# Optimization experiments

Measured on AMD Instinct MI355X. Metric: run time of the kernel, lower is better.

Reference implementation:

```python
import jax, jax.numpy as jnp
import numpy as np

B, QL, D = 4, 1024, 1024
H, HD = 16, 64
KVL = 2048


def setup_inputs() -> dict:
    key = jax.random.key(0)
    ks = jax.random.split(key, 6)
    scale = 1.0 / np.sqrt(D)
    return {
        "hidden_states": jax.random.normal(ks[0], (B, QL, D), dtype=jnp.float32),
        "key_states": jax.random.normal(ks[1], (B, H, KVL, HD), dtype=jnp.float32),
        "value_states": jax.random.normal(ks[2], (B, H, KVL, HD), dtype=jnp.float32),
        "attention_mask": jnp.zeros((B, 1, 1, KVL), dtype=jnp.float32),
        "Wq": jax.random.normal(ks[3], (D, D), dtype=jnp.float32) * scale,
        "Wo": jax.random.normal(ks[4], (D, D), dtype=jnp.float32) * scale,
    }


def reference(hidden_states, key_states, value_states, attention_mask, Wq, Wo):
    batch = hidden_states.shape[0]
    # Q projection (T5 Linear has no bias), split heads: [B, H, Q, HD]
    q = jnp.einsum("bqd,de->bqe", hidden_states, Wq)
    q = q.reshape(batch, -1, H, HD).transpose(0, 2, 1, 3)
    # NOTE: T5 attention has NO 1/sqrt(d) scaling
    scores = jnp.einsum("bhqd,bhkd->bhqk", q, key_states) + attention_mask
    attn = jax.nn.softmax(scores.astype(jnp.float32), axis=-1).astype(scores.dtype)
    out = jnp.einsum("bhqk,bhkd->bhqd", attn, value_states)
    out = out.transpose(0, 2, 1, 3).reshape(batch, -1, H * HD)
    return jnp.einsum("bqe,ed->bqd", out, Wo)
```

## Files before the change

kernel.cpp:

```cpp
#include <hip/hip_runtime.h>
#include <hip/hip_bf16.h>
#include <hip/hip_fp16.h>
#include <stdint.h>

typedef _Float16 f16;
typedef _Float16 f16x2 __attribute__((ext_vector_type(2)));
typedef _Float16 f16x4 __attribute__((ext_vector_type(4)));
typedef _Float16 f16x8 __attribute__((ext_vector_type(8)));
typedef float f32x4 __attribute__((ext_vector_type(4)));
typedef float f32x16 __attribute__((ext_vector_type(16)));

#define B_ 4
#define QL_ 1024
#define D_ 1024
#define H_ 16
#define HD_ 64
#define KVL_ 2048
#define L2E 1.44269504088896f

__device__ __forceinline__ void g2lds16(const void* g, void* l) {
    __builtin_amdgcn_global_load_lds(
        (const __attribute__((address_space(1))) uint32_t*)g,
        (__attribute__((address_space(3))) uint32_t*)l,
        16, 0, 0);
}

union U8 { uint32_t u[4]; f16x8 v; };

__device__ __forceinline__ uint32_t pkrtz(float a, float b) {
    auto t = __builtin_amdgcn_cvt_pkrtz(a, b);
    return __builtin_bit_cast(uint32_t, t);
}

__global__ void preprocess(const float* __restrict__ hs, f16* __restrict__ hs_h,
                           const float* __restrict__ K, f16* __restrict__ K_h,
                           const float* __restrict__ Wq, f16* __restrict__ Wq_t,
                           const float* __restrict__ Wo, f16* __restrict__ Wo_t,
                           const float* __restrict__ V, f16* __restrict__ V_t,
                           const float* __restrict__ mask, float* __restrict__ mL) {
    __shared__ float t[64][65];
    int bid = blockIdx.x, tid = threadIdx.x;
    if (bid < 2048) {
        const int n4a = (B_ * QL_ * D_) / 4;
        const int n4b = (B_ * H_ * KVL_ * HD_) / 4;
        int i = bid * 256 + tid;
        int st = 2048 * 256;
        for (; i < n4a + n4b; i += st) {
            float4 v = (i < n4a) ? ((const float4*)hs)[i] : ((const float4*)K)[i - n4a];
            f16x4 o = { (f16)v.x, (f16)v.y, (f16)v.z, (f16)v.w };
            if (i < n4a) ((f16x4*)hs_h)[i] = o; else ((f16x4*)K_h)[i - n4a] = o;
        }
    } else if (bid < 2560) {
        int wbid = bid - 2048;
        const float* src = wbid < 256 ? Wq : Wo;
        f16* dst = wbid < 256 ? Wq_t : Wo_t;
        int b2 = wbid & 255;
        int k0 = (b2 >> 4) << 6, n0 = (b2 & 15) << 6;
        int rr = tid >> 4, c4 = (tid & 15) << 2;
#pragma unroll
        for (int i = 0; i < 4; ++i) {
            int r = i * 16 + rr;
            float4 v = *(const float4*)(src + (size_t)(k0 + r) * 1024 + n0 + c4);
            t[r][c4 + 0] = v.x; t[r][c4 + 1] = v.y; t[r][c4 + 2] = v.z; t[r][c4 + 3] = v.w;
        }
        __syncthreads();
#pragma unroll
        for (int i = 0; i < 4; ++i) {
            int n = i * 16 + rr;
            f16x4 o;
#pragma unroll
            for (int j = 0; j < 4; ++j) o[j] = (f16)t[c4 + j][n];
            *(f16x4*)(dst + (size_t)(n0 + n) * 1024 + k0 + c4) = o;
        }
    } else if (bid < 4608) {
        int vbid = bid - 2560;
        int bh = vbid >> 5, kv0 = (vbid & 31) << 6;
        int rr = tid >> 4, c4 = (tid & 15) << 2;
        const int permq[4] = {0, 2, 1, 3};
        int pc4 = (c4 & ~15) + permq[(c4 >> 2) & 3] * 4;
#pragma unroll
        for (int i = 0; i < 4; ++i) {
            int r = i * 16 + rr;
            float4 v = *(const float4*)(V + ((size_t)bh * KVL_ + kv0 + r) * HD_ + c4);
            t[r][c4 + 0] = v.x; t[r][c4 + 1] = v.y; t[r][c4 + 2] = v.z; t[r][c4 + 3] = v.w;
        }
        __syncthreads();
#pragma unroll
        for (int i = 0; i < 4; ++i) {
            int d = i * 16 + rr;
            f16x4 o;
#pragma unroll
            for (int j = 0; j < 4; ++j) o[j] = (f16)t[c4 + j][d];
            *(f16x4*)(V_t + ((size_t)bh * HD_ + d) * KVL_ + kv0 + pc4) = o;
        }
    } else {
        int i = (bid - 4608) * 256 + tid;
        if (i < (B_ * KVL_) / 4) {
            f32x4 v = ((const f32x4*)mask)[i];
            v *= L2E;
            ((f32x4*)mL)[i] = v;
        }
    }
}

template <int EPI>
__global__ __launch_bounds__(512) void gemm_tn(
    const f16* __restrict__ A, const f16* __restrict__ BT, void* __restrict__ Cout,
    int M, int N, int K) {
    __shared__ char Alds[2][16384];
    __shared__ char Blds[2][8192];
    int d0 = blockIdx.x;
    int xcd = d0 & 7, sx = d0 >> 3;
    int bm = xcd * 4 + (sx & 3);
    int bn = sx >> 2;
    int tid = threadIdx.x, w = tid >> 6, l = tid & 63;
    int l15 = l & 15, lg = l >> 4;
    int wm = w >> 1, wn = w & 1;
    f32x4 acc[2][2] = {};

    const char* ag[2]; int ao[2];
#pragma unroll
    for (int jj = 0; jj < 2; ++jj) {
        int instr = w + 8 * jj;
        int r = instr * 8 + (l >> 3);
        int cc = (l & 7) ^ (r & 7);
        ag[jj] = (const char*)A + ((size_t)(bm * 128 + r) * K + cc * 8) * 2;
        ao[jj] = instr * 1024;
    }
    int rB = w * 8 + (l >> 3);
    int ccB = (l & 7) ^ (rB & 7);
    const char* bgp = (const char*)BT + ((size_t)(bn * 64 + rB) * K + ccB * 8) * 2;
    int boB = w * 1024;

#define GSTAGE(buf, kt)                                       \
    {                                                         \
        g2lds16(ag[0] + (size_t)(kt) * 128, &Alds[buf][ao[0]]); \
        g2lds16(ag[1] + (size_t)(kt) * 128, &Alds[buf][ao[1]]); \
        g2lds16(bgp + (size_t)(kt) * 128, &Blds[buf][boB]);     \
    }

    int nk = K >> 6;
    GSTAGE(0, 0);
    asm volatile("s_waitcnt vmcnt(0)" ::: "memory");
    __syncthreads();

    for (int kt = 0; kt < nk; ++kt) {
        int cur = kt & 1;
        if (kt + 1 < nk) GSTAGE(cur ^ 1, kt + 1);
#pragma unroll
        for (int ks = 0; ks < 2; ++ks) {
            f16x8 af[2], bf[2];
#pragma unroll
            for (int m = 0; m < 2; ++m) {
                int r = wm * 32 + m * 16 + l15;
                af[m] = *(const f16x8*)(&Alds[cur][r * 128 + ((ks * 64 + lg * 16) ^ ((r & 7) << 4))]);
            }
#pragma unroll
            for (int n = 0; n < 2; ++n) {
                int r = wn * 32 + n * 16 + l15;
                bf[n] = *(const f16x8*)(&Blds[cur][r * 128 + ((ks * 64 + lg * 16) ^ ((r & 7) << 4))]);
            }
#pragma unroll
            for (int m = 0; m < 2; ++m)
#pragma unroll
                for (int n = 0; n < 2; ++n)
                    acc[m][n] = __builtin_amdgcn_mfma_f32_16x16x32_f16(af[m], bf[n], acc[m][n], 0, 0, 0);
        }
        asm volatile("s_waitcnt vmcnt(0)" ::: "memory");
        __syncthreads();
    }

#pragma unroll
    for (int m = 0; m < 2; ++m)
#pragma unroll
        for (int n = 0; n < 2; ++n)
#pragma unroll
            for (int i = 0; i < 4; ++i) {
                int row = bm * 128 + wm * 32 + m * 16 + lg * 4 + i;
                int col = bn * 64 + wn * 32 + n * 16 + l15;
                if (EPI == 0) {
                    float v = acc[m][n][i] * L2E;
                    int b = row >> 10, q = row & 1023, h = col >> 6, d = col & 63;
                    ((f16*)Cout)[(((size_t)b * H_ + h) * QL_ + q) * HD_ + d] = (f16)v;
                } else {
                    ((float*)Cout)[(size_t)row * N + col] = acc[m][n][i];
                }
            }
#undef GSTAGE
}

__global__ __launch_bounds__(512, 4) void attn_fused(
    const f16* __restrict__ qh, const f16* __restrict__ kh, const f16* __restrict__ vt,
    const float* __restrict__ mL, f16* __restrict__ aout) {
    __shared__ char lds_buf[65536];
    __shared__ float frl[8][32];
    __shared__ float fr2[4][2][32];
    __shared__ float2 msx[4][32];

    int tid = threadIdx.x, w = tid >> 6, l = tid & 63;
    int l31 = l & 31, hi = l >> 5;
    int swl = (l31 & 7) << 4;
    int g = w >> 2, wg = w & 3;
    int d0 = blockIdx.x;
    int xcd = d0 & 7, sx = d0 >> 3;
    int bh = xcd * 8 + (sx & 7);
    int qt = sx >> 3;
    int b = bh >> 4, h = bh & 15;

    char* Kst = lds_buf + g * 32768;
    char* Vst = lds_buf + g * 32768 + 16384;

    f16x8 Qf[4];
    {
        const f16* qp = qh + ((size_t)bh * QL_ + qt * 128 + wg * 32 + l31) * HD_ + hi * 8;
#pragma unroll
        for (int ds_ = 0; ds_ < 4; ++ds_) Qf[ds_] = *(const f16x8*)(qp + ds_ * 16);
    }

    const char* kg0; const char* vg0; int ko0, vo0;
    {
        int instr = wg;
        int r = instr * 8 + (l >> 3);
        int cc = (l & 7) ^ (r & 7);
        kg0 = (const char*)kh + ((size_t)bh * KVL_ + g * 1024 + r) * 128 + cc * 16;
        ko0 = instr * 1024;
        vg0 = (const char*)vt + ((size_t)bh * HD_ + r) * (KVL_ * 2) + g * 2048 + cc * 16;
        vo0 = instr * 1024;
    }

#define ASTAGE(buf, ch)                                                              \
    {                                                                                \
        g2lds16(kg0 + (size_t)(ch) * 8192, Kst + (buf) * 8192 + ko0);                \
        g2lds16(kg0 + (size_t)(ch) * 8192 + 4096, Kst + (buf) * 8192 + ko0 + 4096);  \
        g2lds16(vg0 + (size_t)(ch) * 128, Vst + (buf) * 8192 + vo0);                 \
        g2lds16(vg0 + (size_t)(ch) * 128 + 131072, Vst + (buf) * 8192 + vo0 + 4096); \
    }

    float mrun = -1e30f, ssum = 0.f;
    f32x16 acc[2] = {};
    const float* mpb = mL + b * KVL_ + g * 1024;
    const f16x2 one2 = { (f16)1.0f, (f16)1.0f };

    ASTAGE(0, 0);
    asm volatile("s_waitcnt vmcnt(0)" ::: "memory");
    __syncthreads();

    for (int ch = 0; ch < 16; ++ch) {
        int cur = ch & 1;
        if (ch + 1 < 16) ASTAGE(cur ^ 1, ch + 1);
        const char* Kc = Kst + cur * 8192;
        const char* Vc = Vst + cur * 8192;

#pragma unroll
        for (int kb = 0; kb < 2; ++kb) {
            f32x16 St;
#pragma unroll
            for (int g4 = 0; g4 < 4; ++g4) {
                f32x4 mv = *(const f32x4*)(mpb + ch * 64 + kb * 32 + g4 * 8 + hi * 4);
                St[g4 * 4 + 0] = mv[0]; St[g4 * 4 + 1] = mv[1];
                St[g4 * 4 + 2] = mv[2]; St[g4 * 4 + 3] = mv[3];
            }
            __builtin_amdgcn_s_setprio(1);
#pragma unroll
            for (int ds_ = 0; ds_ < 4; ++ds_) {
                f16x8 kf = *(const f16x8*)(Kc + (kb * 32 + l31) * 128 + ((ds_ * 32 + hi * 16) ^ swl));
                St = __builtin_amdgcn_mfma_f32_32x32x16_f16(kf, Qf[ds_], St, 0, 0, 0);
            }
            __builtin_amdgcn_s_setprio(0);

            float a0 = fmaxf(fmaxf(St[0], St[1]), St[2]);
            float a1 = fmaxf(fmaxf(St[3], St[4]), St[5]);
            float a2 = fmaxf(fmaxf(St[6], St[7]), St[8]);
            float a3 = fmaxf(fmaxf(St[9], St[10]), St[11]);
            float a4 = fmaxf(fmaxf(St[12], St[13]), St[14]);
            float pm = fmaxf(fmaxf(fmaxf(a0, a1), St[15]), fmaxf(fmaxf(a2, a3), a4));
            pm = fmaxf(pm, __shfl_xor(pm, 32));

            if (__any(pm > mrun + 12.f)) {
                float mn = fmaxf(mrun, pm);
                float fac = exp2f(mrun - mn);
                mrun = mn;
                ssum *= fac;
                frl[w][l31] = fac;
                asm volatile("s_waitcnt lgkmcnt(0)" ::: "memory");
#pragma unroll
                for (int g4 = 0; g4 < 4; ++g4) {
                    f32x4 fv = *(const f32x4*)&frl[w][g4 * 8 + hi * 4];
#pragma unroll
                    for (int c = 0; c < 2; ++c)
#pragma unroll
                        for (int j = 0; j < 4; ++j) acc[c][g4 * 4 + j] *= fv[j];
                }
            }

            uint32_t pk[8];
#pragma unroll
            for (int i = 0; i < 8; ++i) {
                float p0 = exp2f(St[2 * i] - mrun);
                float p1 = exp2f(St[2 * i + 1] - mrun);
                uint32_t u = pkrtz(p0, p1);
                pk[i] = u;
                ssum = __builtin_amdgcn_fdot2(__builtin_bit_cast(f16x2, u), one2, ssum, false);
            }

            __builtin_amdgcn_s_setprio(1);
#pragma unroll
            for (int sti = 0; sti < 2; ++sti) {
                U8 pa;
                pa.u[0] = pk[sti * 4 + 0]; pa.u[1] = pk[sti * 4 + 1];
                pa.u[2] = pk[sti * 4 + 2]; pa.u[3] = pk[sti * 4 + 3];
                int st_ = kb * 2 + sti;
#pragma unroll
                for (int c = 0; c < 2; ++c) {
                    U8 vb;
                    vb.v = *(const f16x8*)(Vc + (c * 32 + l31) * 128 + ((st_ * 32 + hi * 16) ^ swl));
                    acc[c] = __builtin_amdgcn_mfma_f32_32x32x16_f16(pa.v, vb.v, acc[c], 0, 0, 0);
                }
            }
            __builtin_amdgcn_s_setprio(0);
        }
        asm volatile("s_waitcnt vmcnt(0)" ::: "memory");
        __syncthreads();
    }

    ssum += __shfl_xor(ssum, 32);
    char* exch = lds_buf;
    if (g == 1) {
        int base = (wg * 64 + l) * 128;
#pragma unroll
        for (int i = 0; i < 8; ++i) {
            int c = i >> 2, j0 = (i & 3) * 4;
            f32x4 vv = { acc[c][j0], acc[c][j0 + 1], acc[c][j0 + 2], acc[c][j0 + 3] };
            *(f32x4*)(exch + base + ((i * 16) ^ ((l & 7) << 4))) = vv;
        }
        if (hi == 0) msx[wg][l31] = make_float2(mrun, ssum);
    }
    __syncthreads();
    if (g == 0) {
        float2 mb = msx[wg][l31];
        float m = fmaxf(mrun, mb.x);
        float fA = exp2f(mrun - m), fB = exp2f(mb.x - m);
        float s = ssum * fA + mb.y * fB;
        float rinv = 1.0f / s;
        if (hi == 0) { fr2[wg][0][l31] = fA * rinv; fr2[wg][1][l31] = fB * rinv; }
        asm volatile("s_waitcnt lgkmcnt(0)" ::: "memory");
        int base = (wg * 64 + l) * 128;
#pragma unroll
        for (int c = 0; c < 2; ++c)
#pragma unroll
            for (int g4 = 0; g4 < 4; ++g4) {
                f32x4 gAv = *(const f32x4*)&fr2[wg][0][g4 * 8 + hi * 4];
                f32x4 gBv = *(const f32x4*)&fr2[wg][1][g4 * 8 + hi * 4];
                int i = c * 4 + g4;
                f32x4 pv = *(const f32x4*)(exch + base + ((i * 16) ^ ((l & 7) << 4)));
#pragma unroll
                for (int j = 0; j < 4; ++j) {
                    float o = acc[c][g4 * 4 + j] * gAv[j] + pv[j] * gBv[j];
                    int q = qt * 128 + wg * 32 + g4 * 8 + hi * 4 + j;
                    int dd = c * 32 + l31;
                    aout[((size_t)b * QL_ + q) * D_ + h * HD_ + dd] = (f16)o;
                }
            }
    }
#undef ASTAGE
}

extern "C" void kernel_launch(void* const* d_in, const int* in_sizes, int n_in,
                              void* d_out, int out_size, void* d_ws, size_t ws_size,
                              hipStream_t stream) {
    const float* hs = (const float*)d_in[0];
    const float* K  = (const float*)d_in[1];
    const float* V  = (const float*)d_in[2];
    const float* mask = (const float*)d_in[3];
    const float* Wq = (const float*)d_in[4];
    const float* Wo = (const float*)d_in[5];
    float* out = (float*)d_out;
    char* ws = (char*)d_ws;

    f16* hs_h = (f16*)(ws + 0);
    f16* Wq_t = (f16*)(ws + 8388608);
    f16* Wo_t = (f16*)(ws + 10485760);
    f16* K_h  = (f16*)(ws + 12582912);
    f16* V_t  = (f16*)(ws + 29360128);
    f16* q_h  = (f16*)(ws + 46137344);
    f16* a_o  = (f16*)(ws + 54525952);
    float* mL = (float*)(ws + 62914560);

    preprocess<<<4616, 256, 0, stream>>>(hs, hs_h, K, K_h, Wq, Wq_t, Wo, Wo_t,
                                         V, V_t, mask, mL);
    gemm_tn<0><<<512, 512, 0, stream>>>(hs_h, Wq_t, (void*)q_h, 4096, 1024, 1024);
    attn_fused<<<512, 512, 0, stream>>>(q_h, K_h, V_t, mL, a_o);
    gemm_tn<1><<<512, 512, 0, stream>>>(a_o, Wo_t, (void*)out, 4096, 1024, 1024);
}
```

Before: 117.6 us.

## Pre-swizzle K and V into fragment-ordered layout; unroll GEMM and attention loops

```diff
diff --git a/kernel.cpp b/kernel.cpp
--- a/kernel.cpp
+++ b/kernel.cpp
@@ -40,18 +40,30 @@
                            const float* __restrict__ mask, float* __restrict__ mL) {
     __shared__ float t[64][65];
     int bid = blockIdx.x, tid = threadIdx.x;
-    if (bid < 2048) {
-        const int n4a = (B_ * QL_ * D_) / 4;
-        const int n4b = (B_ * H_ * KVL_ * HD_) / 4;
-        int i = bid * 256 + tid;
-        int st = 2048 * 256;
-        for (; i < n4a + n4b; i += st) {
-            float4 v = (i < n4a) ? ((const float4*)hs)[i] : ((const float4*)K)[i - n4a];
+    if (bid < 1024) {
+        const int n4 = (B_ * QL_ * D_) / 4;
+        for (int i = bid * 256 + tid; i < n4; i += 1024 * 256) {
+            float4 v = ((const float4*)hs)[i];
             f16x4 o = { (f16)v.x, (f16)v.y, (f16)v.z, (f16)v.w };
-            if (i < n4a) ((f16x4*)hs_h)[i] = o; else ((f16x4*)K_h)[i - n4a] = o;
-        }
-    } else if (bid < 2560) {
-        int wbid = bid - 2048;
+            ((f16x4*)hs_h)[i] = o;
+        }
+    } else if (bid < 3072) {
+        int t0 = (bid - 1024) * 256 + tid;
+#pragma unroll
+        for (int rep = 0; rep < 2; ++rep) {
+            int U = t0 + rep * 524288;
+            int bh = U >> 14, rem = U & 16383;
+            int ch = rem >> 9, r2 = rem & 511;
+            int dsl = r2 >> 7, r3 = r2 & 127;
+            int kv = r3 >> 1, hi2 = r3 & 1;
+            const float* sp = K + (((size_t)bh * KVL_ + ch * 64 + kv) * HD_ + dsl * 16 + hi2 * 8);
+            f16x8 o;
+#pragma unroll
+            for (int j = 0; j < 8; ++j) o[j] = (f16)sp[j];
+            *(f16x8*)(K_h + (size_t)U * 8) = o;
+        }
+    } else if (bid < 3584) {
+        int wbid = bid - 3072;
         const float* src = wbid < 256 ? Wq : Wo;
         f16* dst = wbid < 256 ? Wq_t : Wo_t;
         int b2 = wbid & 255;
@@ -72,29 +84,31 @@
             for (int j = 0; j < 4; ++j) o[j] = (f16)t[c4 + j][n];
             *(f16x4*)(dst + (size_t)(n0 + n) * 1024 + k0 + c4) = o;
         }
-    } else if (bid < 4608) {
-        int vbid = bid - 2560;
-        int bh = vbid >> 5, kv0 = (vbid & 31) << 6;
+    } else if (bid < 5632) {
+        int vb = bid - 3584;
+        int bh = vb >> 5, ch = vb & 31;
         int rr = tid >> 4, c4 = (tid & 15) << 2;
-        const int permq[4] = {0, 2, 1, 3};
-        int pc4 = (c4 & ~15) + permq[(c4 >> 2) & 3] * 4;
 #pragma unroll
         for (int i = 0; i < 4; ++i) {
             int r = i * 16 + rr;
-            float4 v = *(const float4*)(V + ((size_t)bh * KVL_ + kv0 + r) * HD_ + c4);
+            float4 v = *(const float4*)(V + ((size_t)bh * KVL_ + ch * 64 + r) * HD_ + c4);
             t[r][c4 + 0] = v.x; t[r][c4 + 1] = v.y; t[r][c4 + 2] = v.z; t[r][c4 + 3] = v.w;
         }
         __syncthreads();
 #pragma unroll
-        for (int i = 0; i < 4; ++i) {
-            int d = i * 16 + rr;
-            f16x4 o;
-#pragma unroll
-            for (int j = 0; j < 4; ++j) o[j] = (f16)t[c4 + j][d];
-            *(f16x4*)(V_t + ((size_t)bh * HD_ + d) * KVL_ + kv0 + pc4) = o;
+        for (int rep = 0; rep < 2; ++rep) {
+            int u = tid + rep * 256;
+            int st = u >> 7, d = (u >> 1) & 63, hi2 = u & 1;
+            f16x8 o;
+#pragma unroll
+            for (int j = 0; j < 8; ++j) {
+                int kvl = st * 16 + (j & 3) + 8 * (j >> 2) + 4 * hi2;
+                o[j] = (f16)t[kvl][d];
+            }
+            *(f16x8*)(V_t + ((size_t)(bh * 32 + ch) * 512 + u) * 8) = o;
         }
     } else {
-        int i = (bid - 4608) * 256 + tid;
+        int i = (bid - 5632) * 256 + tid;
         if (i < (B_ * KVL_) / 4) {
             f32x4 v = ((const f32x4*)mask)[i];
             v *= L2E;
@@ -118,56 +132,65 @@
     int wm = w >> 1, wn = w & 1;
     f32x4 acc[2][2] = {};
 
-    const char* ag[2]; int ao[2];
-#pragma unroll
-    for (int jj = 0; jj < 2; ++jj) {
-        int instr = w + 8 * jj;
-        int r = instr * 8 + (l >> 3);
-        int cc = (l & 7) ^ (r & 7);
-        ag[jj] = (const char*)A + ((size_t)(bm * 128 + r) * K + cc * 8) * 2;
-        ao[jj] = instr * 1024;
+    const char* ag0; const char* ag1; int ao0, ao1;
+    {
+        int i0 = w, i1 = w + 8;
+        int r0 = i0 * 8 + (l >> 3), r1 = i1 * 8 + (l >> 3);
+        int c0 = (l & 7) ^ (r0 & 7), c1 = (l & 7) ^ (r1 & 7);
+        ag0 = (const char*)A + ((size_t)(bm * 128 + r0) * K + c0 * 8) * 2;
+        ag1 = (const char*)A + ((size_t)(bm * 128 + r1) * K + c1 * 8) * 2;
+        ao0 = i0 * 1024; ao1 = i1 * 1024;
     }
     int rB = w * 8 + (l >> 3);
     int ccB = (l & 7) ^ (rB & 7);
     const char* bgp = (const char*)BT + ((size_t)(bn * 64 + rB) * K + ccB * 8) * 2;
     int boB = w * 1024;
 
-#define GSTAGE(buf, kt)                                       \
-    {                                                         \
-        g2lds16(ag[0] + (size_t)(kt) * 128, &Alds[buf][ao[0]]); \
-        g2lds16(ag[1] + (size_t)(kt) * 128, &Alds[buf][ao[1]]); \
-        g2lds16(bgp + (size_t)(kt) * 128, &Blds[buf][boB]);     \
-    }
-
-    int nk = K >> 6;
+    int aoff[2][2], boff[2][2];
+#pragma unroll
+    for (int ks = 0; ks < 2; ++ks)
+#pragma unroll
+        for (int m = 0; m < 2; ++m) {
+            int ra = wm * 32 + m * 16 + l15;
+            aoff[ks][m] = ra * 128 + ((ks * 64 + lg * 16) ^ ((ra & 7) << 4));
+            int rb = wn * 32 + m * 16 + l15;
+            boff[ks][m] = rb * 128 + ((ks * 64 + lg * 16) ^ ((rb & 7) << 4));
+        }
+    const char* Ab = &Alds[0][0];
+    const char* Bb = &Blds[0][0];
+
+#define GSTAGE(buf, soff)                                      \
+    {                                                          \
+        g2lds16(ag0 + (soff), &Alds[buf][ao0]);                \
+        g2lds16(ag1 + (soff), &Alds[buf][ao1]);                \
+        g2lds16(bgp + (soff), &Blds[buf][boB]);                \
+    }
+#define GCOMP(buf)                                                               \
+    _Pragma("unroll") for (int ks = 0; ks < 2; ++ks) {                           \
+        f16x8 af[2], bf[2];                                                      \
+        af[0] = *(const f16x8*)(Ab + (buf) * 16384 + aoff[ks][0]);               \
+        af[1] = *(const f16x8*)(Ab + (buf) * 16384 + aoff[ks][1]);               \
+        bf[0] = *(const f16x8*)(Bb + (buf) * 8192 + boff[ks][0]);                \
+        bf[1] = *(const f16x8*)(Bb + (buf) * 8192 + boff[ks][1]);                \
+        _Pragma("unroll") for (int m = 0; m < 2; ++m)                            \
+            _Pragma("unroll") for (int n = 0; n < 2; ++n)                        \
+                acc[m][n] = __builtin_amdgcn_mfma_f32_16x16x32_f16(af[m], bf[n], acc[m][n], 0, 0, 0); \
+    }
+
     GSTAGE(0, 0);
     asm volatile("s_waitcnt vmcnt(0)" ::: "memory");
     __syncthreads();
 
-    for (int kt = 0; kt < nk; ++kt) {
-        int cur = kt & 1;
-        if (kt + 1 < nk) GSTAGE(cur ^ 1, kt + 1);
-#pragma unroll
-        for (int ks = 0; ks < 2; ++ks) {
-            f16x8 af[2], bf[2];
-#pragma unroll
-            for (int m = 0; m < 2; ++m) {
-                int r = wm * 32 + m * 16 + l15;
-                af[m] = *(const f16x8*)(&Alds[cur][r * 128 + ((ks * 64 + lg * 16) ^ ((r & 7) << 4))]);
-            }
-#pragma unroll
-            for (int n = 0; n < 2; ++n) {
-                int r = wn * 32 + n * 16 + l15;
-                bf[n] = *(const f16x8*)(&Blds[cur][r * 128 + ((ks * 64 + lg * 16) ^ ((r & 7) << 4))]);
-            }
-#pragma unroll
-            for (int m = 0; m < 2; ++m)
-#pragma unroll
-                for (int n = 0; n < 2; ++n)
-                    acc[m][n] = __builtin_amdgcn_mfma_f32_16x16x32_f16(af[m], bf[n], acc[m][n], 0, 0, 0);
-        }
+    for (int t2 = 0; t2 < 8; ++t2) {
+        GSTAGE(1, 128);
+        GCOMP(0);
         asm volatile("s_waitcnt vmcnt(0)" ::: "memory");
         __syncthreads();
+        if (t2 < 7) GSTAGE(0, 256);
+        GCOMP(1);
+        asm volatile("s_waitcnt vmcnt(0)" ::: "memory");
+        __syncthreads();
+        ag0 += 256; ag1 += 256; bgp += 256;
     }
 
 #pragma unroll
@@ -187,6 +210,7 @@
                 }
             }
 #undef GSTAGE
+#undef GCOMP
 }
 
 __global__ __launch_bounds__(512, 4) void attn_fused(
@@ -199,7 +223,6 @@
 
     int tid = threadIdx.x, w = tid >> 6, l = tid & 63;
     int l31 = l & 31, hi = l >> 5;
-    int swl = (l31 & 7) << 4;
     int g = w >> 2, wg = w & 3;
     int d0 = blockIdx.x;
     int xcd = d0 & 7, sx = d0 >> 3;
@@ -207,8 +230,7 @@
     int qt = sx >> 3;
     int b = bh >> 4, h = bh & 15;
 
-    char* Kst = lds_buf + g * 32768;
-    char* Vst = lds_buf + g * 32768 + 16384;
+    const char* lbase = lds_buf + g * 32768 + l31 * 32 + hi * 16;
 
     f16x8 Qf[4];
     {
@@ -217,110 +239,101 @@
         for (int ds_ = 0; ds_ < 4; ++ds_) Qf[ds_] = *(const f16x8*)(qp + ds_ * 16);
     }
 
-    const char* kg0; const char* vg0; int ko0, vo0;
-    {
-        int instr = wg;
-        int r = instr * 8 + (l >> 3);
-        int cc = (l & 7) ^ (r & 7);
-        kg0 = (const char*)kh + ((size_t)bh * KVL_ + g * 1024 + r) * 128 + cc * 16;
-        ko0 = instr * 1024;
-        vg0 = (const char*)vt + ((size_t)bh * HD_ + r) * (KVL_ * 2) + g * 2048 + cc * 16;
-        vo0 = instr * 1024;
-    }
-
-#define ASTAGE(buf, ch)                                                              \
-    {                                                                                \
-        g2lds16(kg0 + (size_t)(ch) * 8192, Kst + (buf) * 8192 + ko0);                \
-        g2lds16(kg0 + (size_t)(ch) * 8192 + 4096, Kst + (buf) * 8192 + ko0 + 4096);  \
-        g2lds16(vg0 + (size_t)(ch) * 128, Vst + (buf) * 8192 + vo0);                 \
-        g2lds16(vg0 + (size_t)(ch) * 128 + 131072, Vst + (buf) * 8192 + vo0 + 4096); \
+    int i0 = wg * 2;
+    const char* kgp0 = (const char*)kh + (((size_t)(bh * 32 + g * 16) * 512) + i0 * 64 + l) * 16;
+    const char* kgp1 = kgp0 + 1024;
+    const char* vgp0 = (const char*)vt + (((size_t)(bh * 32 + g * 16) * 512) + i0 * 64 + l) * 16;
+    const char* vgp1 = vgp0 + 1024;
+    char* kl0 = lds_buf + g * 32768 + i0 * 1024;
+    char* kl1 = kl0 + 1024;
+    char* vl0 = lds_buf + g * 32768 + 16384 + i0 * 1024;
+    char* vl1 = vl0 + 1024;
+
+#define PREF(buf, soff)                                  \
+    {                                                    \
+        g2lds16(kgp0 + (soff), kl0 + (buf) * 8192);      \
+        g2lds16(kgp1 + (soff), kl1 + (buf) * 8192);      \
+        g2lds16(vgp0 + (soff), vl0 + (buf) * 8192);      \
+        g2lds16(vgp1 + (soff), vl1 + (buf) * 8192);      \
     }
 
     float mrun = -1e30f, ssum = 0.f;
     f32x16 acc[2] = {};
-    const float* mpb = mL + b * KVL_ + g * 1024;
+    const float* mp = mL + b * KVL_ + g * 1024;
     const f16x2 one2 = { (f16)1.0f, (f16)1.0f };
 
-    ASTAGE(0, 0);
+#define BODY(buf, mo)                                                                     \
+    _Pragma("unroll") for (int kb = 0; kb < 2; ++kb) {                                    \
+        f32x16 St;                                                                        \
+        _Pragma("unroll") for (int g4 = 0; g4 < 4; ++g4) {                                \
+            f32x4 mv = *(const f32x4*)(mp + (mo) + kb * 32 + g4 * 8 + hi * 4);            \
+            St[g4 * 4 + 0] = mv[0]; St[g4 * 4 + 1] = mv[1];                               \
+            St[g4 * 4 + 2] = mv[2]; St[g4 * 4 + 3] = mv[3];                               \
+        }                                                                                 \
+        __builtin_amdgcn_s_setprio(1);                                                    \
+        _Pragma("unroll") for (int ds_ = 0; ds_ < 4; ++ds_) {                             \
+            f16x8 kf = *(const f16x8*)(lbase + (buf) * 8192 + ds_ * 2048 + kb * 1024);    \
+            St = __builtin_amdgcn_mfma_f32_32x32x16_f16(kf, Qf[ds_], St, 0, 0, 0);        \
+        }                                                                                 \
+        __builtin_amdgcn_s_setprio(0);                                                    \
+        float a0 = fmaxf(fmaxf(St[0], St[1]), St[2]);                                     \
+        float a1 = fmaxf(fmaxf(St[3], St[4]), St[5]);                                     \
+        float a2 = fmaxf(fmaxf(St[6], St[7]), St[8]);                                     \
+        float a3 = fmaxf(fmaxf(St[9], St[10]), St[11]);                                   \
+        float a4 = fmaxf(fmaxf(St[12], St[13]), St[14]);                                  \
+        float pm = fmaxf(fmaxf(fmaxf(a0, a1), St[15]), fmaxf(fmaxf(a2, a3), a4));         \
+        pm = fmaxf(pm, __shfl_xor(pm, 32));                                               \
+        if (__any(pm > mrun + 12.f)) {                                                    \
+            float mn = fmaxf(mrun, pm);                                                   \
+            float fac = exp2f(mrun - mn);                                                 \
+            mrun = mn; ssum *= fac;                                                       \
+            frl[w][l31] = fac;                                                            \
+            asm volatile("s_waitcnt lgkmcnt(0)" ::: "memory");                            \
+            _Pragma("unroll") for (int g4 = 0; g4 < 4; ++g4) {                            \
+                f32x4 fv = *(const f32x4*)&frl[w][g4 * 8 + hi * 4];                       \
+                _Pragma("unroll") for (int c = 0; c < 2; ++c)                             \
+                    _Pragma("unroll") for (int j = 0; j < 4; ++j)                         \
+                        acc[c][g4 * 4 + j] *= fv[j];                                      \
+            }                                                                             \
+        }                                                                                 \
+        uint32_t pk[8];                                                                   \
+        _Pragma("unroll") for (int i = 0; i < 8; ++i) {                                   \
+            float p0 = exp2f(St[2 * i] - mrun);                                           \
+            float p1 = exp2f(St[2 * i + 1] - mrun);                                       \
+            uint32_t u = pkrtz(p0, p1);                                                   \
+            pk[i] = u;                                                                    \
+            ssum = __builtin_amdgcn_fdot2(__builtin_bit_cast(f16x2, u), one2, ssum, false); \
+        }                                                                                 \
+        __builtin_amdgcn_s_setprio(1);                                                    \
+        _Pragma("unroll") for (int sti = 0; sti < 2; ++sti) {                             \
+            U8 pa;                                                                        \
+            pa.u[0] = pk[sti * 4 + 0]; pa.u[1] = pk[sti * 4 + 1];                         \
+            pa.u[2] = pk[sti * 4 + 2]; pa.u[3] = pk[sti * 4 + 3];                         \
+            const int st_ = kb * 2 + sti;                                                 \
+            _Pragma("unroll") for (int c = 0; c < 2; ++c) {                               \
+                U8 vb;                                                                    \
+                vb.v = *(const f16x8*)(lbase + 16384 + (buf) * 8192 + st_ * 2048 + c * 1024); \
+                acc[c] = __builtin_amdgcn_mfma_f32_32x32x16_f16(pa.v, vb.v, acc[c], 0, 0, 0); \
+            }                                                                             \
+        }                                                                                 \
+        __builtin_amdgcn_s_setprio(0);                                                    \
+    }
+
+    PREF(0, 0);
     asm volatile("s_waitcnt vmcnt(0)" ::: "memory");
     __syncthreads();
 
-    for (int ch = 0; ch < 16; ++ch) {
-        int cur = ch & 1;
-        if (ch + 1 < 16) ASTAGE(cur ^ 1, ch + 1);
-        const char* Kc = Kst + cur * 8192;
-        const char* Vc = Vst + cur * 8192;
-
-#pragma unroll
-        for (int kb = 0; kb < 2; ++kb) {
-            f32x16 St;
-#pragma unroll
-            for (int g4 = 0; g4 < 4; ++g4) {
-                f32x4 mv = *(const f32x4*)(mpb + ch * 64 + kb * 32 + g4 * 8 + hi * 4);
-                St[g4 * 4 + 0] = mv[0]; St[g4 * 4 + 1] = mv[1];
-                St[g4 * 4 + 2] = mv[2]; St[g4 * 4 + 3] = mv[3];
-            }
-            __builtin_amdgcn_s_setprio(1);
-#pragma unroll
-            for (int ds_ = 0; ds_ < 4; ++ds_) {
-                f16x8 kf = *(const f16x8*)(Kc + (kb * 32 + l31) * 128 + ((ds_ * 32 + hi * 16) ^ swl));
-                St = __builtin_amdgcn_mfma_f32_32x32x16_f16(kf, Qf[ds_], St, 0, 0, 0);
-            }
-            __builtin_amdgcn_s_setprio(0);
-
-            float a0 = fmaxf(fmaxf(St[0], St[1]), St[2]);
-            float a1 = fmaxf(fmaxf(St[3], St[4]), St[5]);
-            float a2 = fmaxf(fmaxf(St[6], St[7]), St[8]);
-            float a3 = fmaxf(fmaxf(St[9], St[10]), St[11]);
-            float a4 = fmaxf(fmaxf(St[12], St[13]), St[14]);
-            float pm = fmaxf(fmaxf(fmaxf(a0, a1), St[15]), fmaxf(fmaxf(a2, a3), a4));
-            pm = fmaxf(pm, __shfl_xor(pm, 32));
-
-            if (__any(pm > mrun + 12.f)) {
-                float mn = fmaxf(mrun, pm);
-                float fac = exp2f(mrun - mn);
-                mrun = mn;
-                ssum *= fac;
-                frl[w][l31] = fac;
-                asm volatile("s_waitcnt lgkmcnt(0)" ::: "memory");
-#pragma unroll
-                for (int g4 = 0; g4 < 4; ++g4) {
-                    f32x4 fv = *(const f32x4*)&frl[w][g4 * 8 + hi * 4];
-#pragma unroll
-                    for (int c = 0; c < 2; ++c)
-#pragma unroll
-                        for (int j = 0; j < 4; ++j) acc[c][g4 * 4 + j] *= fv[j];
-                }
-            }
-
-            uint32_t pk[8];
-#pragma unroll
-            for (int i = 0; i < 8; ++i) {
-                float p0 = exp2f(St[2 * i] - mrun);
-                float p1 = exp2f(St[2 * i + 1] - mrun);
-                uint32_t u = pkrtz(p0, p1);
-                pk[i] = u;
-                ssum = __builtin_amdgcn_fdot2(__builtin_bit_cast(f16x2, u), one2, ssum, false);
-            }
-
-            __builtin_amdgcn_s_setprio(1);
-#pragma unroll
-            for (int sti = 0; sti < 2; ++sti) {
-                U8 pa;
-                pa.u[0] = pk[sti * 4 + 0]; pa.u[1] = pk[sti * 4 + 1];
-                pa.u[2] = pk[sti * 4 + 2]; pa.u[3] = pk[sti * 4 + 3];
-                int st_ = kb * 2 + sti;
-#pragma unroll
-                for (int c = 0; c < 2; ++c) {
-                    U8 vb;
-                    vb.v = *(const f16x8*)(Vc + (c * 32 + l31) * 128 + ((st_ * 32 + hi * 16) ^ swl));
-                    acc[c] = __builtin_amdgcn_mfma_f32_32x32x16_f16(pa.v, vb.v, acc[c], 0, 0, 0);
-                }
-            }
-            __builtin_amdgcn_s_setprio(0);
-        }
+    for (int it = 0; it < 8; ++it) {
+        PREF(1, 8192);
+        BODY(0, 0);
         asm volatile("s_waitcnt vmcnt(0)" ::: "memory");
         __syncthreads();
+        if (it < 7) PREF(0, 16384);
+        BODY(1, 64);
+        asm volatile("s_waitcnt vmcnt(0)" ::: "memory");
+        __syncthreads();
+        kgp0 += 16384; kgp1 += 16384; vgp0 += 16384; vgp1 += 16384;
+        mp += 128;
     }
 
     ssum += __shfl_xor(ssum, 32);
@@ -362,7 +375,8 @@
                 }
             }
     }
-#undef ASTAGE
+#undef PREF
+#undef BODY
 }
 
 extern "C" void kernel_launch(void* const* d_in, const int* in_sizes, int n_in,
@@ -386,7 +400,7 @@
     f16* a_o  = (f16*)(ws + 54525952);
     float* mL = (float*)(ws + 62914560);
 
-    preprocess<<<4616, 256, 0, stream>>>(hs, hs_h, K, K_h, Wq, Wq_t, Wo, Wo_t,
+    preprocess<<<5640, 256, 0, stream>>>(hs, hs_h, K, K_h, Wq, Wq_t, Wo, Wo_t,
                                          V, V_t, mask, mL);
     gemm_tn<0><<<512, 512, 0, stream>>>(hs_h, Wq_t, (void*)q_h, 4096, 1024, 1024);
     attn_fused<<<512, 512, 0, stream>>>(q_h, K_h, V_t, mL, a_o);
```

Result: no change. 117.4 us (-0.1%).
